# Performance work log

Measured on AMD Instinct MI355X. Metric: run time of the kernel, lower is better.

The kernel has to match this reference:

```python
import jax, jax.numpy as jnp
import numpy as np

D_MODEL = 1024
NHEAD = 16
D_K = D_MODEL // NHEAD
SPARSITY = 0.9
DROP_P = 0.1


def setup_inputs() -> dict:
    key = jax.random.key(0)
    ks = jax.random.split(key, 11)
    B, S = 4, 2048
    s = 1.0 / np.sqrt(D_MODEL)
    return {
        "query": jax.random.normal(ks[0], (B, S, D_MODEL), jnp.float32),
        "key": jax.random.normal(ks[1], (B, S, D_MODEL), jnp.float32),
        "value": jax.random.normal(ks[2], (B, S, D_MODEL), jnp.float32),
        "Wq": jax.random.normal(ks[3], (D_MODEL, D_MODEL), jnp.float32) * s,
        "bq": jnp.zeros((D_MODEL,), jnp.float32),
        "Wk": jax.random.normal(ks[4], (D_MODEL, D_MODEL), jnp.float32) * s,
        "bk": jnp.zeros((D_MODEL,), jnp.float32),
        "Wv": jax.random.normal(ks[5], (D_MODEL, D_MODEL), jnp.float32) * s,
        "bv": jnp.zeros((D_MODEL,), jnp.float32),
        "Wo": jax.random.normal(ks[6], (D_MODEL, D_MODEL), jnp.float32) * s,
        "bo": jnp.zeros((D_MODEL,), jnp.float32),
    }


def reference(query, key, value, Wq, bq, Wk, bk, Wv, bv, Wo, bo):
    B, S, _ = query.shape
    # torch Linear: x @ W.T + b
    def proj(x, W, b):
        return (x @ W.T + b).reshape(B, S, NHEAD, D_K).transpose(0, 2, 1, 3)

    Q = proj(query, Wq, bq)   # [B,H,S,d_k]
    K = proj(key, Wk, bk)
    V = proj(value, Wv, bv)

    scores = jnp.einsum("bhqd,bhkd->bhqk", Q, K) / jnp.sqrt(jnp.float32(D_K))
    # random sparsity mask: keep where rand > sparsity (fixed RNG key)
    mkey = jax.random.key(42)
    keep = jax.random.uniform(mkey, scores.shape, jnp.float32) > SPARSITY
    scores = jnp.where(keep, scores, -jnp.inf)
    probs = jax.nn.softmax(scores, axis=-1)
    # dropout on attention probs (train mode, inverted dropout)
    dkey = jax.random.key(7)
    dmask = jax.random.bernoulli(dkey, 1.0 - DROP_P, probs.shape)
    probs = probs * dmask / (1.0 - DROP_P)

    out = jnp.einsum("bhqk,bhkd->bhqd", probs, V)  # [B,H,S,d_k]
    out = out.transpose(0, 2, 1, 3).reshape(B, S, D_MODEL)
    return out @ Wo.T + bo
```

## Files before the change

kernel.cpp:

```cpp
#include <hip/hip_runtime.h>
#include <stdint.h>

typedef unsigned short u16;
typedef unsigned int u32;
typedef __attribute__((ext_vector_type(8))) short short8;
typedef __attribute__((ext_vector_type(4))) float f32x4;

#define DEVI static __device__ __forceinline__

#define S_LEN 2048
#define DMODEL 1024
#define NHEAD 16
#define DK 64
#define NEG_INF (-__builtin_inff())
#define KEEPC 3865470976u
#define DROPC 3865470464u

DEVI u16 f2bf(float f) {
  u32 u = __builtin_bit_cast(u32, f);
  u32 r = u + 0x7fffu + ((u >> 16) & 1u);
  return (u16)(r >> 16);
}

DEVI short8 cvt8(float4 a, float4 b) {
  short8 r;
  r[0] = (short)f2bf(a.x); r[1] = (short)f2bf(a.y);
  r[2] = (short)f2bf(a.z); r[3] = (short)f2bf(a.w);
  r[4] = (short)f2bf(b.x); r[5] = (short)f2bf(b.y);
  r[6] = (short)f2bf(b.z); r[7] = (short)f2bf(b.w);
  return r;
}

DEVI u32 tf_bits(u32 key, u32 i) {
  const u32 K2 = key ^ 0x1BD11BDAu;
  u32 x0 = 0u, x1 = i + key;
#define TFR(r) { x0 += x1; x1 = __builtin_rotateleft32(x1, r); x1 ^= x0; }
  TFR(13) TFR(15) TFR(26) TFR(6)  x0 += key; x1 += K2 + 1u;
  TFR(17) TFR(29) TFR(16) TFR(24) x0 += K2;  x1 += 2u;
  TFR(13) TFR(15) TFR(26) TFR(6)    x1 += key + 3u;
  TFR(17) TFR(29) TFR(16) TFR(24) x0 += key; x1 += K2 + 4u;
  TFR(13) TFR(15) TFR(26) TFR(6)  x0 += K2;  x1 += 5u;
#undef TFR
  return x0 ^ x1;
}

__global__ __launch_bounds__(256) void proj_kernel(
    const float* __restrict__ Xq, const float* __restrict__ Xk, const float* __restrict__ Xv,
    const float* __restrict__ Wq, const float* __restrict__ Wk, const float* __restrict__ Wv,
    const float* __restrict__ bq, const float* __restrict__ bk, const float* __restrict__ bv,
    u16* __restrict__ Qo, u16* __restrict__ Ko, u16* __restrict__ Vto)
{
  const int z = blockIdx.z;
  const float* X = (z == 0) ? Xq : (z == 1) ? Xk : Xv;
  const float* W = (z == 0) ? Wq : (z == 1) ? Wk : Wv;
  const float* bias = (z == 0) ? bq : (z == 1) ? bk : bv;
  const int m0 = blockIdx.x * 64, n0 = blockIdx.y * 64;
  const int tid = threadIdx.x, w = tid >> 6, lane = tid & 63, l = lane & 15, quad = lane >> 4;

  __shared__ __align__(16) u16 lsA[2048], lsB[2048];

  const int srow = tid >> 2, skp = tid & 3;
  const int sc = ((srow >> 4) * 64 + skp * 16 + (srow & 15)) * 8;
  const float* gA = X + (u32)(m0 + srow) * DMODEL + skp * 8;
  const float* gB = W + (u32)(n0 + srow) * DMODEL + skp * 8;

  f32x4 acc[2][2] = {};
  const int mh = (w >> 1) * 2, nh = (w & 1) * 2;

  for (int k0 = 0; k0 < DMODEL; k0 += 32) {
    short8 av  = cvt8(*(const float4*)(gA + k0), *(const float4*)(gA + k0 + 4));
    short8 bv8 = cvt8(*(const float4*)(gB + k0), *(const float4*)(gB + k0 + 4));
    __syncthreads();
    *(short8*)(lsA + sc) = av;
    *(short8*)(lsB + sc) = bv8;
    __syncthreads();
    short8 a0 = *(const short8*)(lsA + ((mh + 0) * 64 + lane) * 8);
    short8 a1 = *(const short8*)(lsA + ((mh + 1) * 64 + lane) * 8);
    short8 b0 = *(const short8*)(lsB + ((nh + 0) * 64 + lane) * 8);
    short8 b1 = *(const short8*)(lsB + ((nh + 1) * 64 + lane) * 8);
    acc[0][0] = __builtin_amdgcn_mfma_f32_16x16x32_bf16(a0, b0, acc[0][0], 0, 0, 0);
    acc[0][1] = __builtin_amdgcn_mfma_f32_16x16x32_bf16(a0, b1, acc[0][1], 0, 0, 0);
    acc[1][0] = __builtin_amdgcn_mfma_f32_16x16x32_bf16(a1, b0, acc[1][0], 0, 0, 0);
    acc[1][1] = __builtin_amdgcn_mfma_f32_16x16x32_bf16(a1, b1, acc[1][1], 0, 0, 0);
  }

  #pragma unroll
  for (int ma = 0; ma < 2; ++ma) {
    #pragma unroll
    for (int nb = 0; nb < 2; ++nb) {
      const int n = n0 + (nh + nb) * 16 + l;
      const float bval = bias[n];
      const int h = n >> 6, d = n & 63;
      #pragma unroll
      for (int r = 0; r < 4; ++r) {
        const int m = m0 + (mh + ma) * 16 + quad * 4 + r;
        float val = acc[ma][nb][r] + bval;
        if (z == 0) val *= 0.125f;
        const int b = m >> 11, s = m & 2047;
        if (z == 0)      Qo [((u32)(b * NHEAD + h) * S_LEN + s) * DK + d] = f2bf(val);
        else if (z == 1) Ko [((u32)(b * NHEAD + h) * S_LEN + s) * DK + d] = f2bf(val);
        else             Vto[((u32)(b * NHEAD + h) * DK + d) * S_LEN + s] = f2bf(val);
      }
    }
  }
}

__global__ __launch_bounds__(256) void attn_kernel(
    const u16* __restrict__ Qs, const u16* __restrict__ Ks, const u16* __restrict__ Vts,
    u16* __restrict__ ctx)
{
  const int qb = blockIdx.x, bh = blockIdx.y;
  const int tid = threadIdx.x, w = tid >> 6, lane = tid & 63, l = lane & 15, quad = lane >> 4;

  __shared__ __align__(16) u16 Kf[4096];
  __shared__ __align__(16) u16 Vf[4096];
  __shared__ __align__(16) u16 Pf[4][1024];

  const int qrow0 = qb * 64 + w * 16;
  const u32 qbase = (u32)(bh * S_LEN + qrow0 + l) * DK + quad * 8;
  const short8 qa0 = *(const short8*)(Qs + qbase);
  const short8 qa1 = *(const short8*)(Qs + qbase + 32);

  u32 ibase = ((u32)bh * 2048u + (u32)(qrow0 + quad * 4)) * 2048u + (u32)l;

  f32x4 o[4] = {};
  float mr[4] = {NEG_INF, NEG_INF, NEG_INF, NEG_INF};
  float lr[4] = {0.f, 0.f, 0.f, 0.f};

  const int tA = tid, tB = tid + 256;
  const int keyA = tA >> 3, dpA = tA & 7;
  const int kcA = (((dpA >> 2) * 4 + (keyA >> 4)) * 64 + (dpA & 3) * 16 + (keyA & 15)) * 8;
  const u32 gkA = (u32)(bh * S_LEN + keyA) * DK + dpA * 8;
  const int keyB = tB >> 3, dpB = tB & 7;
  const int kcB = (((dpB >> 2) * 4 + (keyB >> 4)) * 64 + (dpB & 3) * 16 + (keyB & 15)) * 8;
  const u32 gkB = (u32)(bh * S_LEN + keyB) * DK + dpB * 8;
  const int vcA = (((keyA >> 4) * 2 + (dpA >> 2)) * 64 + (dpA & 3) * 16 + (keyA & 15)) * 8;
  const u32 gvA = (u32)(bh * DK + keyA) * S_LEN + dpA * 8;
  const int vcB = (((keyB >> 4) * 2 + (dpB >> 2)) * 64 + (dpB & 3) * 16 + (keyB & 15)) * 8;
  const u32 gvB = (u32)(bh * DK + keyB) * S_LEN + dpB * 8;

  for (int kt = 0; kt < 32; ++kt) {
    const u32 ko = (u32)kt * 64u;
    short8 k0v = *(const short8*)(Ks + gkA + ko * DK);
    short8 k1v = *(const short8*)(Ks + gkB + ko * DK);
    short8 v0v = *(const short8*)(Vts + gvA + ko);
    short8 v1v = *(const short8*)(Vts + gvB + ko);

    u32 m16 = 0;
    #pragma unroll
    for (int c = 0; c < 4; ++c) {
      #pragma unroll
      for (int r = 0; r < 4; ++r) {
        m16 |= (u32)(tf_bits(42u, ibase + (u32)(r * 2048 + c * 16)) >= KEEPC) << (c * 4 + r);
      }
    }
    u32 d16 = 0, mm = m16;
    while (mm) {
      const u32 s = (u32)__builtin_ctz(mm); mm &= mm - 1u;
      const u32 ii = ibase + (s & 3u) * 2048u + (s >> 2) * 16u;
      d16 |= (u32)(tf_bits(7u, ii) < DROPC) << s;
    }
    ibase += 64u;

    __syncthreads();
    *(short8*)(Kf + kcA) = k0v;
    *(short8*)(Kf + kcB) = k1v;
    *(short8*)(Vf + vcA) = v0v;
    *(short8*)(Vf + vcB) = v1v;
    __syncthreads();

    f32x4 sc4[4];
    #pragma unroll
    for (int nc = 0; nc < 4; ++nc) {
      short8 kb0 = *(const short8*)(Kf + (nc * 64 + lane) * 8);
      short8 kb1 = *(const short8*)(Kf + ((4 + nc) * 64 + lane) * 8);
      f32x4 zz = {0.f, 0.f, 0.f, 0.f};
      zz = __builtin_amdgcn_mfma_f32_16x16x32_bf16(qa0, kb0, zz, 0, 0, 0);
      sc4[nc] = __builtin_amdgcn_mfma_f32_16x16x32_bf16(qa1, kb1, zz, 0, 0, 0);
    }

    u16* pw = Pf[w];
    #pragma unroll
    for (int r = 0; r < 4; ++r) {
      float v0 = ((m16 >> (r + 0))  & 1u) ? sc4[0][r] : NEG_INF;
      float v1 = ((m16 >> (r + 4))  & 1u) ? sc4[1][r] : NEG_INF;
      float v2 = ((m16 >> (r + 8))  & 1u) ? sc4[2][r] : NEG_INF;
      float v3 = ((m16 >> (r + 12)) & 1u) ? sc4[3][r] : NEG_INF;
      float mx = fmaxf(fmaxf(v0, v1), fmaxf(v2, v3));
      mx = fmaxf(mx, __shfl_xor(mx, 1));
      mx = fmaxf(mx, __shfl_xor(mx, 2));
      mx = fmaxf(mx, __shfl_xor(mx, 4));
      mx = fmaxf(mx, __shfl_xor(mx, 8));
      const float mn = fmaxf(mr[r], mx);
      const float alpha = (mn == NEG_INF) ? 1.f : __expf(mr[r] - mn);
      mr[r] = mn;
      const float p0 = (v0 == NEG_INF) ? 0.f : __expf(v0 - mn);
      const float p1 = (v1 == NEG_INF) ? 0.f : __expf(v1 - mn);
      const float p2 = (v2 == NEG_INF) ? 0.f : __expf(v2 - mn);
      const float p3 = (v3 == NEG_INF) ? 0.f : __expf(v3 - mn);
      float rs = p0 + p1 + p2 + p3;
      rs += __shfl_xor(rs, 1);
      rs += __shfl_xor(rs, 2);
      rs += __shfl_xor(rs, 4);
      rs += __shfl_xor(rs, 8);
      lr[r] = alpha * lr[r] + rs;
      o[0][r] = o[0][r] * alpha; o[1][r] = o[1][r] * alpha;
      o[2][r] = o[2][r] * alpha; o[3][r] = o[3][r] * alpha;
      const float pd0 = ((d16 >> (r + 0))  & 1u) ? p0 * (1.f / 0.9f) : 0.f;
      const float pd1 = ((d16 >> (r + 4))  & 1u) ? p1 * (1.f / 0.9f) : 0.f;
      const float pd2 = ((d16 >> (r + 8))  & 1u) ? p2 * (1.f / 0.9f) : 0.f;
      const float pd3 = ((d16 >> (r + 12)) & 1u) ? p3 * (1.f / 0.9f) : 0.f;
      const int hi = l >> 3, bq_ = quad * 4 + r, j = l & 7;
      pw[((hi) * 16 + bq_) * 8 + j]            = f2bf(pd0);
      pw[((2 + hi) * 16 + bq_) * 8 + j]        = f2bf(pd1);
      pw[(64 + hi * 16 + bq_) * 8 + j]         = f2bf(pd2);
      pw[(64 + (2 + hi) * 16 + bq_) * 8 + j]   = f2bf(pd3);
    }
    short8 pa0 = *(const short8*)(Pf[w] + lane * 8);
    short8 pa1 = *(const short8*)(Pf[w] + (64 + lane) * 8);
    #pragma unroll
    for (int nd = 0; nd < 4; ++nd) {
      short8 vb0 = *(const short8*)(Vf + ((nd * 2 + 0) * 64 + lane) * 8);
      short8 vb1 = *(const short8*)(Vf + ((nd * 2 + 1) * 64 + lane) * 8);
      o[nd] = __builtin_amdgcn_mfma_f32_16x16x32_bf16(pa0, vb0, o[nd], 0, 0, 0);
      o[nd] = __builtin_amdgcn_mfma_f32_16x16x32_bf16(pa1, vb1, o[nd], 0, 0, 0);
    }
  }

  const int b = bh >> 4, h = bh & 15;
  #pragma unroll
  for (int r = 0; r < 4; ++r) {
    const float inv = 1.f / lr[r];
    const int qrow = qb * 64 + w * 16 + quad * 4 + r;
    const u32 ob = (u32)(b * S_LEN + qrow) * DMODEL + h * DK;
    ctx[ob + 0  + l] = f2bf(o[0][r] * inv);
    ctx[ob + 16 + l] = f2bf(o[1][r] * inv);
    ctx[ob + 32 + l] = f2bf(o[2][r] * inv);
    ctx[ob + 48 + l] = f2bf(o[3][r] * inv);
  }
}

__global__ __launch_bounds__(256) void oproj_kernel(
    const u16* __restrict__ X, const float* __restrict__ W, const float* __restrict__ bias,
    float* __restrict__ out)
{
  const int m0 = blockIdx.x * 64, n0 = blockIdx.y * 64;
  const int tid = threadIdx.x, w = tid >> 6, lane = tid & 63, l = lane & 15, quad = lane >> 4;

  __shared__ __align__(16) u16 lsA[2048], lsB[2048];

  const int srow = tid >> 2, skp = tid & 3;
  const int sc = ((srow >> 4) * 64 + skp * 16 + (srow & 15)) * 8;
  const u16*  gA = X + (u32)(m0 + srow) * DMODEL + skp * 8;
  const float* gB = W + (u32)(n0 + srow) * DMODEL + skp * 8;

  f32x4 acc[2][2] = {};
  const int mh = (w >> 1) * 2, nh = (w & 1) * 2;

  for (int k0 = 0; k0 < DMODEL; k0 += 32) {
    short8 av  = *(const short8*)(gA + k0);
    short8 bv8 = cvt8(*(const float4*)(gB + k0), *(const float4*)(gB + k0 + 4));
    __syncthreads();
    *(short8*)(lsA + sc) = av;
    *(short8*)(lsB + sc) = bv8;
    __syncthreads();
    short8 a0 = *(const short8*)(lsA + ((mh + 0) * 64 + lane) * 8);
    short8 a1 = *(const short8*)(lsA + ((mh + 1) * 64 + lane) * 8);
    short8 b0 = *(const short8*)(lsB + ((nh + 0) * 64 + lane) * 8);
    short8 b1 = *(const short8*)(lsB + ((nh + 1) * 64 + lane) * 8);
    acc[0][0] = __builtin_amdgcn_mfma_f32_16x16x32_bf16(a0, b0, acc[0][0], 0, 0, 0);
    acc[0][1] = __builtin_amdgcn_mfma_f32_16x16x32_bf16(a0, b1, acc[0][1], 0, 0, 0);
    acc[1][0] = __builtin_amdgcn_mfma_f32_16x16x32_bf16(a1, b0, acc[1][0], 0, 0, 0);
    acc[1][1] = __builtin_amdgcn_mfma_f32_16x16x32_bf16(a1, b1, acc[1][1], 0, 0, 0);
  }

  #pragma unroll
  for (int ma = 0; ma < 2; ++ma) {
    #pragma unroll
    for (int nb = 0; nb < 2; ++nb) {
      const int n = n0 + (nh + nb) * 16 + l;
      const float bval = bias[n];
      #pragma unroll
      for (int r = 0; r < 4; ++r) {
        const int m = m0 + (mh + ma) * 16 + quad * 4 + r;
        out[(u32)m * DMODEL + n] = acc[ma][nb][r] + bval;
      }
    }
  }
}

extern "C" void kernel_launch(void* const* d_in, const int* in_sizes, int n_in,
                              void* d_out, int out_size, void* d_ws, size_t ws_size,
                              hipStream_t stream) {
  (void)in_sizes; (void)n_in; (void)out_size; (void)ws_size;
  const float* q  = (const float*)d_in[0];
  const float* k  = (const float*)d_in[1];
  const float* v  = (const float*)d_in[2];
  const float* Wq = (const float*)d_in[3];
  const float* bq = (const float*)d_in[4];
  const float* Wk = (const float*)d_in[5];
  const float* bk = (const float*)d_in[6];
  const float* Wv = (const float*)d_in[7];
  const float* bv = (const float*)d_in[8];
  const float* Wo = (const float*)d_in[9];
  const float* bo = (const float*)d_in[10];

  char* ws = (char*)d_ws;
  u16* Qs   = (u16*)(ws);
  u16* Ks   = (u16*)(ws + 16777216);
  u16* Vts  = (u16*)(ws + 33554432);
  u16* ctx  = (u16*)(ws + 50331648);

  proj_kernel<<<dim3(128, 16, 3), 256, 0, stream>>>(q, k, v, Wq, Wk, Wv,
                                                    bq, bk, bv, Qs, Ks, Vts);
  attn_kernel<<<dim3(32, 64), 256, 0, stream>>>(Qs, Ks, Vts, ctx);
  oproj_kernel<<<dim3(128, 16), 256, 0, stream>>>(ctx, Wo, bo, (float*)d_out);
}
```

Baseline: 1.162 ms.

## Alias P staging buffer onto K tile in LDS and swizzle P writes

Removes the separate per-wave P buffer and reuses the K shared-memory tile for the probabilities after an extra barrier, which cuts LDS per block to allow more resident blocks. Launch bounds now request 8 blocks per CU. The P write and read indices are XOR-swizzled to reduce LDS bank conflicts. The added barrier per tile and the tighter register budget from the launch bound could offset the gain.

```diff
diff --git a/kernel.cpp b/kernel.cpp
--- a/kernel.cpp
+++ b/kernel.cpp
@@ -105,16 +105,15 @@
   }
 }
 
-__global__ __launch_bounds__(256) void attn_kernel(
+__global__ __launch_bounds__(256, 8) void attn_kernel(
     const u16* __restrict__ Qs, const u16* __restrict__ Ks, const u16* __restrict__ Vts,
     u16* __restrict__ ctx)
 {
   const int qb = blockIdx.x, bh = blockIdx.y;
   const int tid = threadIdx.x, w = tid >> 6, lane = tid & 63, l = lane & 15, quad = lane >> 4;
 
-  __shared__ __align__(16) u16 Kf[4096];
+  __shared__ __align__(16) u16 KPf[4096];
   __shared__ __align__(16) u16 Vf[4096];
-  __shared__ __align__(16) u16 Pf[4][1024];
 
   const int qrow0 = qb * 64 + w * 16;
   const u32 qbase = (u32)(bh * S_LEN + qrow0 + l) * DK + quad * 8;
@@ -139,6 +138,12 @@
   const int vcB = (((keyB >> 4) * 2 + (dpB >> 2)) * 64 + (dpB & 3) * 16 + (keyB & 15)) * 8;
   const u32 gvB = (u32)(bh * DK + keyB) * S_LEN + dpB * 8;
 
+  const int hi = l >> 3, j = l & 7;
+  const int pxor = ((quad >> 1) << 3) | (hi << 4);
+  const int pb = (hi * 128 + quad * 32 + j) ^ pxor;
+  const int prd = (lane * 8) ^ (lane & 24);
+  u16* const pw = KPf + w * 1024;
+
   for (int kt = 0; kt < 32; ++kt) {
     const u32 ko = (u32)kt * 64u;
     short8 k0v = *(const short8*)(Ks + gkA + ko * DK);
@@ -163,8 +168,8 @@
     ibase += 64u;
 
     __syncthreads();
-    *(short8*)(Kf + kcA) = k0v;
-    *(short8*)(Kf + kcB) = k1v;
+    *(short8*)(KPf + kcA) = k0v;
+    *(short8*)(KPf + kcB) = k1v;
     *(short8*)(Vf + vcA) = v0v;
     *(short8*)(Vf + vcB) = v1v;
     __syncthreads();
@@ -172,14 +177,15 @@
     f32x4 sc4[4];
     #pragma unroll
     for (int nc = 0; nc < 4; ++nc) {
-      short8 kb0 = *(const short8*)(Kf + (nc * 64 + lane) * 8);
-      short8 kb1 = *(const short8*)(Kf + ((4 + nc) * 64 + lane) * 8);
+      short8 kb0 = *(const short8*)(KPf + (nc * 64 + lane) * 8);
+      short8 kb1 = *(const short8*)(KPf + ((4 + nc) * 64 + lane) * 8);
       f32x4 zz = {0.f, 0.f, 0.f, 0.f};
       zz = __builtin_amdgcn_mfma_f32_16x16x32_bf16(qa0, kb0, zz, 0, 0, 0);
-      sc4[nc] = __builtin_amdgcn_mfma_f32_16x16x32_bf16(qa1, kb1, zz, 0, 0, 0);
-    }
-
-    u16* pw = Pf[w];
+      sc4[nc] = __builtin_amdgcn_mfma_f32_16x16x32_bf16(qa1, kb1, sc4[nc] = zz, 0, 0, 0);
+    }
+
+    __syncthreads();
+
     #pragma unroll
     for (int r = 0; r < 4; ++r) {
       float v0 = ((m16 >> (r + 0))  & 1u) ? sc4[0][r] : NEG_INF;
@@ -210,14 +216,14 @@
       const float pd1 = ((d16 >> (r + 4))  & 1u) ? p1 * (1.f / 0.9f) : 0.f;
       const float pd2 = ((d16 >> (r + 8))  & 1u) ? p2 * (1.f / 0.9f) : 0.f;
       const float pd3 = ((d16 >> (r + 12)) & 1u) ? p3 * (1.f / 0.9f) : 0.f;
-      const int hi = l >> 3, bq_ = quad * 4 + r, j = l & 7;
-      pw[((hi) * 16 + bq_) * 8 + j]            = f2bf(pd0);
-      pw[((2 + hi) * 16 + bq_) * 8 + j]        = f2bf(pd1);
-      pw[(64 + hi * 16 + bq_) * 8 + j]         = f2bf(pd2);
-      pw[(64 + (2 + hi) * 16 + bq_) * 8 + j]   = f2bf(pd3);
-    }
-    short8 pa0 = *(const short8*)(Pf[w] + lane * 8);
-    short8 pa1 = *(const short8*)(Pf[w] + (64 + lane) * 8);
+      const int pi = pb ^ (r * 8);
+      pw[pi      ] = f2bf(pd0);
+      pw[pi + 256] = f2bf(pd1);
+      pw[pi + 512] = f2bf(pd2);
+      pw[pi + 768] = f2bf(pd3);
+    }
+    short8 pa0 = *(const short8*)(pw + prd);
+    short8 pa1 = *(const short8*)(pw + 512 + prd);
     #pragma unroll
     for (int nd = 0; nd < 4; ++nd) {
       short8 vb0 = *(const short8*)(Vf + ((nd * 2 + 0) * 64 + lane) * 8);
```

Result: slower. 1.193 ms (+2.7%).
